# Optimization experiments

Measured on AMD Instinct MI355X. Metric: run time of the kernel, lower is better.

Reference implementation:

```python
import jax, jax.numpy as jnp
import numpy as np

BOX = 256
SIGMA = 1.5
KS = 9  # int(ceil(6*sigma)), made odd
N_POINTS = 20000
N_NEURONS = 32
N_LAYERS = 3
LATENT = 8
BATCH = 16


def _make_kernel2(ks, sigma):
    ax = np.arange(ks) - ks // 2
    yy, xx = np.meshgrid(ax, ax, indexing='ij')
    k = np.exp(-(xx ** 2 + yy ** 2) / (2.0 * sigma ** 2))
    return (k / k.sum()).astype(np.float32)


def setup_inputs() -> dict:
    key = jax.random.key(0)
    ks = jax.random.split(key, 16)
    def n(k, shape, scale=1.0):
        return scale * jax.random.normal(k, shape, dtype=jnp.float32)
    return {
        'z': n(ks[0], (BATCH, LATENT)),
        'r': n(ks[1], (BATCH, 3, 3)),
        'pos': 0.1 * (jax.random.uniform(ks[2], (N_POINTS, 3), dtype=jnp.float32) - 0.5),
        'amp': 0.1 * jnp.ones((1,), jnp.float32),
        'linamp1_W': n(ks[3], (N_NEURONS, 4), 0.3),
        'ampblock_W': n(ks[4], (N_LAYERS, N_NEURONS, N_NEURONS), 0.1),
        'ampblock_b': n(ks[5], (N_LAYERS, N_NEURONS), 0.05),
        'linamp2_W': n(ks[6], (1, N_NEURONS), 0.1),
        'linamp2_b': n(ks[7], (1,), 0.05),
        'lin0_W': n(ks[8], (N_NEURONS, 3 + LATENT - 1), 0.3),
        'deform_W': n(ks[9], (N_LAYERS, N_NEURONS, N_NEURONS), 0.1),
        'deform_b': n(ks[10], (N_LAYERS, N_NEURONS), 0.05),
        'lin1a_W': n(ks[11], (3, N_NEURONS), 0.2),
        'lin1b_W': n(ks[12], (3, 3), 0.2),
        'k2': jnp.asarray(_make_kernel2(KS, SIGMA)),
        'd': 1,
    }


def _res_mlp(x, Ws, bs):
    # residual blocks: x <- relu(x @ W^T + b) + x
    for i in range(Ws.shape[0]):
        x = jax.nn.relu(x @ Ws[i].T + bs[i]) + x
    return x


def _splat(proj, amps, k2):
    # Gaussian-kernel splat of points onto [B, BOX, BOX] images.
    # proj: [B,P,2] coords in ~[-0.5, 0.5]; amps: [B,P]; k2: [KS,KS]
    B, P, _ = proj.shape
    ks = k2.shape[0]
    half = ks // 2
    pix = (proj + 0.5) * (BOX - 1)
    cx = jnp.round(pix[..., 0]).astype(jnp.int32)
    cy = jnp.round(pix[..., 1]).astype(jnp.int32)
    offs = jnp.arange(ks, dtype=jnp.int32) - half
    oy, ox = jnp.meshgrid(offs, offs, indexing='ij')
    xx = cx[:, :, None] + ox.reshape(-1)[None, None, :]   # [B,P,ks*ks]
    yy = cy[:, :, None] + oy.reshape(-1)[None, None, :]
    w = amps[:, :, None] * k2.reshape(-1)[None, None, :]
    valid = (xx >= 0) & (xx < BOX) & (yy >= 0) & (yy < BOX)
    bidx = jnp.arange(B, dtype=jnp.int32)[:, None, None]
    flat = jnp.where(valid, (bidx * BOX + yy) * BOX + xx, 0)
    img = jnp.zeros((B * BOX * BOX,), proj.dtype).at[flat.reshape(-1)].add(
        jnp.where(valid, w, jnp.zeros_like(w)).reshape(-1))
    return img.reshape(B, BOX, BOX)


def _forward(z, r, pos, amp, linamp1_W, ampblock_W, ampblock_b, linamp2_W,
             linamp2_b, lin0_W, deform_W, deform_b, lin1a_W, lin1b_W, k2, d):
    B = z.shape[0]
    P = pos.shape[0]
    posi = jnp.broadcast_to(pos[None], (B, P, 3))
    # amplitude head (diff_conf=True): last latent channel per point
    conf_a = jnp.broadcast_to(z[:, -1:][:, None, :], (B, P, 1))
    a = jnp.concatenate([posi, conf_a], axis=-1) @ linamp1_W.T
    a = _res_mlp(a, ampblock_W, ampblock_b)
    amp_corr = jax.nn.sigmoid(a @ linamp2_W.T + linamp2_b)  # [B,P,1]
    # deformation head on remaining latent channels
    if d > 0:
        conf = jnp.broadcast_to(z[:, :-1][:, None, :], (B, P, z.shape[1] - 1))
        res = jnp.concatenate([posi, conf], axis=-1) @ lin0_W.T
        res = _res_mlp(res, deform_W, deform_b)
        res = jnp.tanh(res @ lin1a_W.T)
        res = res @ lin1b_W.T
        pos_def = posi + res
    else:
        res = jnp.zeros_like(posi)
        pos_def = posi
    # project rotated points to 2D
    proj_pos = jnp.einsum('bij,bpj->bpi', r, pos_def)[..., :2]
    amps = amp * amp_corr[..., 0]  # [B,P]
    proj_im = _splat(proj_pos, amps, k2)
    return proj_im, pos_def, res, amp_corr


def reference(z, r, pos, amp, linamp1_W, ampblock_W, ampblock_b, linamp2_W,
              linamp2_b, lin0_W, deform_W, deform_b, lin1a_W, lin1b_W, k2, d):
    return _forward(z, r, pos, amp, linamp1_W, ampblock_W, ampblock_b,
                    linamp2_W, linamp2_b, lin0_W, deform_W, deform_b,
                    lin1a_W, lin1b_W, k2, d)
```

## Files before the change

kernel.cpp:

```cpp
#include <hip/hip_runtime.h>

#define BOX   256
#define KS    9
#define HALF  4
#define NPTS  20000
#define NB    16
#define NLAT  8
#define CANW  264
#define NPBLK 2500
#define CANVAS_ELEMS (NB * CANW * CANW)

typedef _Float16 half8   __attribute__((ext_vector_type(8)));
typedef __fp16   fp16x2  __attribute__((ext_vector_type(2)));
typedef float    floatx4 __attribute__((ext_vector_type(4)));

#define WH_BYTES 16384

__device__ __forceinline__ int perm_inv(int k) {
    return ((k >> 2) & 1) * 16 + (k >> 3) * 4 + (k & 3);
}

__device__ __forceinline__ half8 pack8(const float x[8]) {
    union { fp16x2 v2[4]; half8 v8; } u;
    u.v2[0] = __builtin_amdgcn_cvt_pkrtz(x[0], x[1]);
    u.v2[1] = __builtin_amdgcn_cvt_pkrtz(x[2], x[3]);
    u.v2[2] = __builtin_amdgcn_cvt_pkrtz(x[4], x[5]);
    u.v2[3] = __builtin_amdgcn_cvt_pkrtz(x[6], x[7]);
    return u.v8;
}

__global__ __launch_bounds__(256) void prep_kernel(
    const float* __restrict__ linamp1_W, const float* __restrict__ ampblock_W,
    const float* __restrict__ lin0_W, const float* __restrict__ deform_W,
    _Float16* __restrict__ wh)
{
    const int idx = blockIdx.x * 256 + threadIdx.x;
    if (idx >= 8192) return;
    const int mat = idx >> 10, rem = idx & 1023;
    const int m = rem >> 5, k = rem & 31;
    float v = 0.0f;
    if (mat == 0)      { if (k < 4)  v = linamp1_W[m * 4 + k]; }
    else if (mat <= 3) { v = ampblock_W[(mat - 1) * 1024 + m * 32 + perm_inv(k)]; }
    else if (mat == 4) { if (k < 10) v = lin0_W[m * 10 + k]; }
    else               { v = deform_W[(mat - 5) * 1024 + m * 32 + perm_inv(k)]; }
    wh[idx] = (_Float16)v;
}

__global__ __launch_bounds__(256) void point_kernel(
    const float* __restrict__ z, const float* __restrict__ r,
    const float* __restrict__ pos, const float* __restrict__ amp,
    const float* __restrict__ ampblock_b, const float* __restrict__ linamp2_W,
    const float* __restrict__ linamp2_b, const float* __restrict__ deform_b,
    const float* __restrict__ lin1a_W, const float* __restrict__ lin1b_W,
    const int* __restrict__ dflag, const _Float16* __restrict__ wh,
    float* __restrict__ canvas, float* __restrict__ pos_def_out,
    float* __restrict__ res_out, float* __restrict__ amp_corr_out)
{
    const int lane = threadIdx.x & 63;
    const int n    = lane & 15;
    const int quad = lane >> 4;
    const int aoff = quad * 8;
    const int s    = blockIdx.x * 4 + (threadIdx.x >> 6);
    const int d    = *dflag;
    const float ampv = amp[0];
    const float l2b  = linamp2_b[0];
    const floatx4 zero = {0.f, 0.f, 0.f, 0.f};

    const int base0 = s * 32;
    const int b     = base0 / NPTS;

    float zl[NLAT];
    #pragma unroll
    for (int k = 0; k < NLAT; ++k) zl[k] = z[b * NLAT + k];

    float px[2], py[2], pz[2];
    half8 bfa[2], bfd[2];
    #pragma unroll
    for (int g = 0; g < 2; ++g) {
        const int p = base0 - b * NPTS + g * 16 + n;
        px[g] = pos[3 * p + 0];
        py[g] = pos[3 * p + 1];
        pz[g] = pos[3 * p + 2];
        half8 t;
        #pragma unroll
        for (int j = 0; j < 8; ++j) t[j] = (_Float16)0.f;
        bfa[g] = t; bfd[g] = t;
        if (quad == 0) {
            bfa[g][0] = (_Float16)px[g]; bfa[g][1] = (_Float16)py[g];
            bfa[g][2] = (_Float16)pz[g]; bfa[g][3] = (_Float16)zl[7];
            bfd[g][0] = (_Float16)px[g]; bfd[g][1] = (_Float16)py[g];
            bfd[g][2] = (_Float16)pz[g]; bfd[g][3] = (_Float16)zl[0];
            bfd[g][4] = (_Float16)zl[1]; bfd[g][5] = (_Float16)zl[2];
            bfd[g][6] = (_Float16)zl[3]; bfd[g][7] = (_Float16)zl[4];
        } else if (quad == 1) {
            bfd[g][0] = (_Float16)zl[5]; bfd[g][1] = (_Float16)zl[6];
        }
    }

    float xB[2][8];
    {
        half8 a0 = *(const half8*)(wh + n * 32 + aoff);
        half8 a1 = *(const half8*)(wh + (n + 16) * 32 + aoff);
        #pragma unroll
        for (int g = 0; g < 2; ++g) {
            floatx4 c0 = __builtin_amdgcn_mfma_f32_16x16x32_f16(a0, bfa[g], zero, 0, 0, 0);
            floatx4 c1 = __builtin_amdgcn_mfma_f32_16x16x32_f16(a1, bfa[g], zero, 0, 0, 0);
            #pragma unroll
            for (int rr = 0; rr < 4; ++rr) { xB[g][rr] = c0[rr]; xB[g][4 + rr] = c1[rr]; }
        }
    }
    #pragma unroll
    for (int l = 0; l < 3; ++l) {
        const _Float16* M = wh + (1 + l) * 1024;
        half8 a0 = *(const half8*)(M + n * 32 + aoff);
        half8 a1 = *(const half8*)(M + (n + 16) * 32 + aoff);
        floatx4 b0 = *(const floatx4*)(ampblock_b + l * 32 + quad * 4);
        floatx4 b1 = *(const floatx4*)(ampblock_b + l * 32 + 16 + quad * 4);
        #pragma unroll
        for (int g = 0; g < 2; ++g) {
            half8 hf = pack8(xB[g]);
            floatx4 d0 = __builtin_amdgcn_mfma_f32_16x16x32_f16(a0, hf, b0, 0, 0, 0);
            floatx4 d1 = __builtin_amdgcn_mfma_f32_16x16x32_f16(a1, hf, b1, 0, 0, 0);
            #pragma unroll
            for (int rr = 0; rr < 4; ++rr) {
                xB[g][rr]     += fmaxf(d0[rr], 0.f);
                xB[g][4 + rr] += fmaxf(d1[rr], 0.f);
            }
        }
    }
    float corr[2];
    {
        floatx4 wa = *(const floatx4*)(linamp2_W + quad * 4);
        floatx4 wb = *(const floatx4*)(linamp2_W + 16 + quad * 4);
        #pragma unroll
        for (int g = 0; g < 2; ++g) {
            float sd = 0.f;
            #pragma unroll
            for (int rr = 0; rr < 4; ++rr) sd += wa[rr] * xB[g][rr] + wb[rr] * xB[g][4 + rr];
            sd += __shfl_xor(sd, 16);
            sd += __shfl_xor(sd, 32);
            corr[g] = 1.f / (1.f + __expf(-(sd + l2b)));
        }
    }

    float r0[2] = {0.f, 0.f}, r1[2] = {0.f, 0.f}, r2[2] = {0.f, 0.f};
    if (d > 0) {
        {
            const _Float16* M = wh + 4 * 1024;
            half8 a0 = *(const half8*)(M + n * 32 + aoff);
            half8 a1 = *(const half8*)(M + (n + 16) * 32 + aoff);
            #pragma unroll
            for (int g = 0; g < 2; ++g) {
                floatx4 c0 = __builtin_amdgcn_mfma_f32_16x16x32_f16(a0, bfd[g], zero, 0, 0, 0);
                floatx4 c1 = __builtin_amdgcn_mfma_f32_16x16x32_f16(a1, bfd[g], zero, 0, 0, 0);
                #pragma unroll
                for (int rr = 0; rr < 4; ++rr) { xB[g][rr] = c0[rr]; xB[g][4 + rr] = c1[rr]; }
            }
        }
        #pragma unroll
        for (int l = 0; l < 3; ++l) {
            const _Float16* M = wh + (5 + l) * 1024;
            half8 a0 = *(const half8*)(M + n * 32 + aoff);
            half8 a1 = *(const half8*)(M + (n + 16) * 32 + aoff);
            floatx4 b0 = *(const floatx4*)(deform_b + l * 32 + quad * 4);
            floatx4 b1 = *(const floatx4*)(deform_b + l * 32 + 16 + quad * 4);
            #pragma unroll
            for (int g = 0; g < 2; ++g) {
                half8 hf = pack8(xB[g]);
                floatx4 d0 = __builtin_amdgcn_mfma_f32_16x16x32_f16(a0, hf, b0, 0, 0, 0);
                floatx4 d1 = __builtin_amdgcn_mfma_f32_16x16x32_f16(a1, hf, b1, 0, 0, 0);
                #pragma unroll
                for (int rr = 0; rr < 4; ++rr) {
                    xB[g][rr]     += fmaxf(d0[rr], 0.f);
                    xB[g][4 + rr] += fmaxf(d1[rr], 0.f);
                }
            }
        }
        #pragma unroll
        for (int i = 0; i < 3; ++i) {
            floatx4 wa = *(const floatx4*)(lin1a_W + i * 32 + quad * 4);
            floatx4 wb = *(const floatx4*)(lin1a_W + i * 32 + 16 + quad * 4);
            const float lb0 = lin1b_W[0 * 3 + i];
            const float lb1 = lin1b_W[1 * 3 + i];
            const float lb2 = lin1b_W[2 * 3 + i];
            #pragma unroll
            for (int g = 0; g < 2; ++g) {
                float sd = 0.f;
                #pragma unroll
                for (int rr = 0; rr < 4; ++rr) sd += wa[rr] * xB[g][rr] + wb[rr] * xB[g][4 + rr];
                sd += __shfl_xor(sd, 16);
                sd += __shfl_xor(sd, 32);
                const float t3 = 1.f - 2.f / (__expf(2.f * sd) + 1.f);
                r0[g] = fmaf(t3, lb0, r0[g]);
                r1[g] = fmaf(t3, lb1, r1[g]);
                r2[g] = fmaf(t3, lb2, r2[g]);
            }
        }
    }

    #pragma unroll
    for (int g = 0; g < 2; ++g) {
        const int bp = base0 + g * 16 + n;
        const float pdx = px[g] + r0[g], pdy = py[g] + r1[g], pdz = pz[g] + r2[g];
        if (quad == 0) {
            pos_def_out[3 * bp + 0] = pdx;
            pos_def_out[3 * bp + 1] = pdy;
            pos_def_out[3 * bp + 2] = pdz;
        } else if (quad == 1) {
            res_out[3 * bp + 0] = r0[g];
            res_out[3 * bp + 1] = r1[g];
            res_out[3 * bp + 2] = r2[g];
        } else if (quad == 2) {
            amp_corr_out[bp] = corr[g];
        } else {
            const float* rb = r + b * 9;
            const float pjx = rb[0] * pdx + rb[1] * pdy + rb[2] * pdz;
            const float pjy = rb[3] * pdx + rb[4] * pdy + rb[5] * pdz;
            const int cx = (int)rintf((pjx + 0.5f) * (float)(BOX - 1));
            const int cy = (int)rintf((pjy + 0.5f) * (float)(BOX - 1));
            if (cx >= -HALF && cx <= BOX - 1 + HALF &&
                cy >= -HALF && cy <= BOX - 1 + HALF) {
                atomicAdd(canvas + ((size_t)b * CANW + (cy + HALF)) * CANW + (cx + HALF),
                          ampv * corr[g]);
            }
        }
    }
}

__global__ __launch_bounds__(256) void conv_kernel(
    const float* __restrict__ canvas, const float* __restrict__ k2,
    float* __restrict__ img)
{
    __shared__ float t_lds[24][256];
    const int x  = threadIdx.x;
    const int b  = blockIdx.x >> 4;
    const int y0 = (blockIdx.x & 15) * 16;

    float g[KS];
    #pragma unroll
    for (int i = 0; i < KS; ++i) {
        float sg = 0.f;
        #pragma unroll
        for (int j = 0; j < KS; ++j) sg += k2[i * KS + j];
        g[i] = sg;
    }

    const float* cb = canvas + (size_t)b * CANW * CANW;
    #pragma unroll 4
    for (int rr = 0; rr < 24; ++rr) {
        const float* row = cb + (size_t)(y0 + rr) * CANW;
        float s = 0.f;
        #pragma unroll
        for (int i = 0; i < KS; ++i) s = fmaf(g[i], row[x + (KS - 1) - i], s);
        t_lds[rr][x] = s;
    }
    __syncthreads();

    float* ib = img + ((size_t)b * BOX + y0) * BOX;
    #pragma unroll 4
    for (int yy = 0; yy < 16; ++yy) {
        float s = 0.f;
        #pragma unroll
        for (int i = 0; i < KS; ++i) s = fmaf(g[i], t_lds[yy + (KS - 1) - i][x], s);
        ib[yy * BOX + x] = s;
    }
}

extern "C" void kernel_launch(void* const* d_in, const int* in_sizes, int n_in,
                              void* d_out, int out_size, void* d_ws, size_t ws_size,
                              hipStream_t stream) {
    const float* z          = (const float*)d_in[0];
    const float* r          = (const float*)d_in[1];
    const float* pos        = (const float*)d_in[2];
    const float* amp        = (const float*)d_in[3];
    const float* linamp1_W  = (const float*)d_in[4];
    const float* ampblock_W = (const float*)d_in[5];
    const float* ampblock_b = (const float*)d_in[6];
    const float* linamp2_W  = (const float*)d_in[7];
    const float* linamp2_b  = (const float*)d_in[8];
    const float* lin0_W     = (const float*)d_in[9];
    const float* deform_W   = (const float*)d_in[10];
    const float* deform_b   = (const float*)d_in[11];
    const float* lin1a_W    = (const float*)d_in[12];
    const float* lin1b_W    = (const float*)d_in[13];
    const float* k2         = (const float*)d_in[14];
    const int*   dflag      = (const int*)d_in[15];

    float* out = (float*)d_out;
    float* img          = out;
    float* pos_def_out  = out + (size_t)NB * BOX * BOX;
    float* res_out      = pos_def_out + (size_t)NB * NPTS * 3;
    float* amp_corr_out = res_out + (size_t)NB * NPTS * 3;

    _Float16* wh     = (_Float16*)d_ws;
    float*    canvas = (float*)((char*)d_ws + WH_BYTES);

    (void)hipMemsetAsync(canvas, 0, (size_t)CANVAS_ELEMS * sizeof(float), stream);

    prep_kernel<<<32, 256, 0, stream>>>(
        linamp1_W, ampblock_W, lin0_W, deform_W, wh);

    point_kernel<<<NPBLK, 256, 0, stream>>>(
        z, r, pos, amp, ampblock_b, linamp2_W, linamp2_b, deform_b,
        lin1a_W, lin1b_W, dflag, wh, canvas,
        pos_def_out, res_out, amp_corr_out);

    conv_kernel<<<NB * 16, 256, 0, stream>>>(canvas, k2, img);
}
```

Before: 136.5 us.

## Use MFMA for output heads, merge canvas zeroing into prep kernel

Replaces the per-point dot-product-plus-shuffle reductions for the amplitude head and the deformation output head with small MFMA ops, using new fp16 weight matrices packed in the prep kernel. All outputs are now written by a single quad per point instead of spreading the work across four quads. The canvas memset is folded into the prep kernel, which removes one launch. The cost is extra MFMA issue on mostly zero-padded matrices, fp16 rounding of those weights, and three of four quads sitting idle during the epilogue.

```diff
diff --git a/kernel.cpp b/kernel.cpp
--- a/kernel.cpp
+++ b/kernel.cpp
@@ -9,12 +9,13 @@
 #define CANW  264
 #define NPBLK 2500
 #define CANVAS_ELEMS (NB * CANW * CANW)
+#define CANVAS_F4    (CANVAS_ELEMS / 4)
 
 typedef _Float16 half8   __attribute__((ext_vector_type(8)));
 typedef __fp16   fp16x2  __attribute__((ext_vector_type(2)));
 typedef float    floatx4 __attribute__((ext_vector_type(4)));
 
-#define WH_BYTES 16384
+#define WH_BYTES 20480
 
 __device__ __forceinline__ int perm_inv(int k) {
     return ((k >> 2) & 1) * 16 + (k >> 3) * 4 + (k & 3);
@@ -32,26 +33,35 @@
 __global__ __launch_bounds__(256) void prep_kernel(
     const float* __restrict__ linamp1_W, const float* __restrict__ ampblock_W,
     const float* __restrict__ lin0_W, const float* __restrict__ deform_W,
-    _Float16* __restrict__ wh)
+    const float* __restrict__ linamp2_W, const float* __restrict__ lin1a_W,
+    _Float16* __restrict__ wh, float* __restrict__ canvas)
 {
     const int idx = blockIdx.x * 256 + threadIdx.x;
-    if (idx >= 8192) return;
-    const int mat = idx >> 10, rem = idx & 1023;
-    const int m = rem >> 5, k = rem & 31;
-    float v = 0.0f;
-    if (mat == 0)      { if (k < 4)  v = linamp1_W[m * 4 + k]; }
-    else if (mat <= 3) { v = ampblock_W[(mat - 1) * 1024 + m * 32 + perm_inv(k)]; }
-    else if (mat == 4) { if (k < 10) v = lin0_W[m * 10 + k]; }
-    else               { v = deform_W[(mat - 5) * 1024 + m * 32 + perm_inv(k)]; }
-    wh[idx] = (_Float16)v;
+
+    if (idx < CANVAS_F4) {
+        floatx4 zv = {0.f, 0.f, 0.f, 0.f};
+        ((floatx4*)canvas)[idx] = zv;
+    }
+
+    if (idx < 10 * 1024) {
+        const int mat = idx >> 10, rem = idx & 1023;
+        const int m = rem >> 5, k = rem & 31;
+        float v = 0.0f;
+        if (mat == 0)      { if (k < 4)  v = linamp1_W[m * 4 + k]; }
+        else if (mat <= 3) { v = ampblock_W[(mat - 1) * 1024 + m * 32 + perm_inv(k)]; }
+        else if (mat == 4) { if (k < 10) v = lin0_W[m * 10 + k]; }
+        else if (mat <= 7) { v = deform_W[(mat - 5) * 1024 + m * 32 + perm_inv(k)]; }
+        else if (mat == 8) { if (m == 0) v = linamp2_W[perm_inv(k)]; }
+        else               { if (m < 3)  v = lin1a_W[m * 32 + perm_inv(k)]; }
+        wh[idx] = (_Float16)v;
+    }
 }
 
 __global__ __launch_bounds__(256) void point_kernel(
     const float* __restrict__ z, const float* __restrict__ r,
     const float* __restrict__ pos, const float* __restrict__ amp,
-    const float* __restrict__ ampblock_b, const float* __restrict__ linamp2_W,
-    const float* __restrict__ linamp2_b, const float* __restrict__ deform_b,
-    const float* __restrict__ lin1a_W, const float* __restrict__ lin1b_W,
+    const float* __restrict__ ampblock_b, const float* __restrict__ linamp2_b,
+    const float* __restrict__ deform_b, const float* __restrict__ lin1b_W,
     const int* __restrict__ dflag, const _Float16* __restrict__ wh,
     float* __restrict__ canvas, float* __restrict__ pos_def_out,
     float* __restrict__ res_out, float* __restrict__ amp_corr_out)
@@ -62,8 +72,6 @@
     const int aoff = quad * 8;
     const int s    = blockIdx.x * 4 + (threadIdx.x >> 6);
     const int d    = *dflag;
-    const float ampv = amp[0];
-    const float l2b  = linamp2_b[0];
     const floatx4 zero = {0.f, 0.f, 0.f, 0.f};
 
     const int base0 = s * 32;
@@ -128,22 +136,17 @@
             }
         }
     }
-    float corr[2];
+    floatx4 dA[2];
     {
-        floatx4 wa = *(const floatx4*)(linamp2_W + quad * 4);
-        floatx4 wb = *(const floatx4*)(linamp2_W + 16 + quad * 4);
-        #pragma unroll
-        for (int g = 0; g < 2; ++g) {
-            float sd = 0.f;
-            #pragma unroll
-            for (int rr = 0; rr < 4; ++rr) sd += wa[rr] * xB[g][rr] + wb[rr] * xB[g][4 + rr];
-            sd += __shfl_xor(sd, 16);
-            sd += __shfl_xor(sd, 32);
-            corr[g] = 1.f / (1.f + __expf(-(sd + l2b)));
-        }
-    }
-
-    float r0[2] = {0.f, 0.f}, r1[2] = {0.f, 0.f}, r2[2] = {0.f, 0.f};
+        half8 tA = *(const half8*)(wh + 8 * 1024 + n * 32 + aoff);
+        #pragma unroll
+        for (int g = 0; g < 2; ++g) {
+            half8 hf = pack8(xB[g]);
+            dA[g] = __builtin_amdgcn_mfma_f32_16x16x32_f16(tA, hf, zero, 0, 0, 0);
+        }
+    }
+
+    floatx4 dD[2] = {zero, zero};
     if (d > 0) {
         {
             const _Float16* M = wh + 4 * 1024;
@@ -176,52 +179,54 @@
                 }
             }
         }
-        #pragma unroll
-        for (int i = 0; i < 3; ++i) {
-            floatx4 wa = *(const floatx4*)(lin1a_W + i * 32 + quad * 4);
-            floatx4 wb = *(const floatx4*)(lin1a_W + i * 32 + 16 + quad * 4);
-            const float lb0 = lin1b_W[0 * 3 + i];
-            const float lb1 = lin1b_W[1 * 3 + i];
-            const float lb2 = lin1b_W[2 * 3 + i];
-            #pragma unroll
-            for (int g = 0; g < 2; ++g) {
-                float sd = 0.f;
-                #pragma unroll
-                for (int rr = 0; rr < 4; ++rr) sd += wa[rr] * xB[g][rr] + wb[rr] * xB[g][4 + rr];
-                sd += __shfl_xor(sd, 16);
-                sd += __shfl_xor(sd, 32);
-                const float t3 = 1.f - 2.f / (__expf(2.f * sd) + 1.f);
-                r0[g] = fmaf(t3, lb0, r0[g]);
-                r1[g] = fmaf(t3, lb1, r1[g]);
-                r2[g] = fmaf(t3, lb2, r2[g]);
-            }
-        }
-    }
-
-    #pragma unroll
-    for (int g = 0; g < 2; ++g) {
-        const int bp = base0 + g * 16 + n;
-        const float pdx = px[g] + r0[g], pdy = py[g] + r1[g], pdz = pz[g] + r2[g];
-        if (quad == 0) {
+        half8 tD = *(const half8*)(wh + 9 * 1024 + n * 32 + aoff);
+        #pragma unroll
+        for (int g = 0; g < 2; ++g) {
+            half8 hf = pack8(xB[g]);
+            dD[g] = __builtin_amdgcn_mfma_f32_16x16x32_f16(tD, hf, zero, 0, 0, 0);
+        }
+    }
+
+    if (quad == 0) {
+        const float l2b = linamp2_b[0];
+        const float ampv = amp[0];
+        const float lb0 = lin1b_W[0], lb1 = lin1b_W[1], lb2 = lin1b_W[2];
+        const float lb3 = lin1b_W[3], lb4 = lin1b_W[4], lb5 = lin1b_W[5];
+        const float lb6 = lin1b_W[6], lb7 = lin1b_W[7], lb8 = lin1b_W[8];
+        const float* rb = r + b * 9;
+        const float r00 = rb[0], r01 = rb[1], r02 = rb[2];
+        const float r10 = rb[3], r11 = rb[4], r12 = rb[5];
+        #pragma unroll
+        for (int g = 0; g < 2; ++g) {
+            const int bp = base0 + g * 16 + n;
+            const float corr = 1.f / (1.f + __expf(-(dA[g][0] + l2b)));
+            float r0 = 0.f, r1 = 0.f, r2 = 0.f;
+            if (d > 0) {
+                const float t0 = 1.f - 2.f / (__expf(2.f * dD[g][0]) + 1.f);
+                const float t1 = 1.f - 2.f / (__expf(2.f * dD[g][1]) + 1.f);
+                const float t2 = 1.f - 2.f / (__expf(2.f * dD[g][2]) + 1.f);
+                r0 = t0 * lb0 + t1 * lb1 + t2 * lb2;
+                r1 = t0 * lb3 + t1 * lb4 + t2 * lb5;
+                r2 = t0 * lb6 + t1 * lb7 + t2 * lb8;
+            }
+            const float pdx = px[g] + r0, pdy = py[g] + r1, pdz = pz[g] + r2;
+
             pos_def_out[3 * bp + 0] = pdx;
             pos_def_out[3 * bp + 1] = pdy;
             pos_def_out[3 * bp + 2] = pdz;
-        } else if (quad == 1) {
-            res_out[3 * bp + 0] = r0[g];
-            res_out[3 * bp + 1] = r1[g];
-            res_out[3 * bp + 2] = r2[g];
-        } else if (quad == 2) {
-            amp_corr_out[bp] = corr[g];
-        } else {
-            const float* rb = r + b * 9;
-            const float pjx = rb[0] * pdx + rb[1] * pdy + rb[2] * pdz;
-            const float pjy = rb[3] * pdx + rb[4] * pdy + rb[5] * pdz;
+            res_out[3 * bp + 0] = r0;
+            res_out[3 * bp + 1] = r1;
+            res_out[3 * bp + 2] = r2;
+            amp_corr_out[bp] = corr;
+
+            const float pjx = r00 * pdx + r01 * pdy + r02 * pdz;
+            const float pjy = r10 * pdx + r11 * pdy + r12 * pdz;
             const int cx = (int)rintf((pjx + 0.5f) * (float)(BOX - 1));
             const int cy = (int)rintf((pjy + 0.5f) * (float)(BOX - 1));
             if (cx >= -HALF && cx <= BOX - 1 + HALF &&
                 cy >= -HALF && cy <= BOX - 1 + HALF) {
                 atomicAdd(canvas + ((size_t)b * CANW + (cy + HALF)) * CANW + (cx + HALF),
-                          ampv * corr[g]);
+                          ampv * corr);
             }
         }
     }
@@ -295,15 +300,13 @@
     _Float16* wh     = (_Float16*)d_ws;
     float*    canvas = (float*)((char*)d_ws + WH_BYTES);
 
-    (void)hipMemsetAsync(canvas, 0, (size_t)CANVAS_ELEMS * sizeof(float), stream);
-
-    prep_kernel<<<32, 256, 0, stream>>>(
-        linamp1_W, ampblock_W, lin0_W, deform_W, wh);
+    prep_kernel<<<(CANVAS_F4 + 255) / 256, 256, 0, stream>>>(
+        linamp1_W, ampblock_W, lin0_W, deform_W, linamp2_W, lin1a_W,
+        wh, canvas);
 
     point_kernel<<<NPBLK, 256, 0, stream>>>(
-        z, r, pos, amp, ampblock_b, linamp2_W, linamp2_b, deform_b,
-        lin1a_W, lin1b_W, dflag, wh, canvas,
-        pos_def_out, res_out, amp_corr_out);
+        z, r, pos, amp, ampblock_b, linamp2_b, deform_b, lin1b_W,
+        dflag, wh, canvas, pos_def_out, res_out, amp_corr_out);
 
     conv_kernel<<<NB * 16, 256, 0, stream>>>(canvas, k2, img);
 }
```

After: 139.4 us. 2.1% more time.
